# Performance work log

Measured on AMD Instinct MI355X. Metric: run time of the kernel, lower is better.

Reference implementation:

```python
import jax, jax.numpy as jnp
import numpy as np

B, CIN, H, W = 16, 3, 128, 128
C = 256          # out_channels
NH = 8           # num_heads
HD = C // NH     # head_dim = 32
SCALE = HD ** -0.5
EPS = 1e-5


def setup_inputs() -> dict:
    key = jax.random.key(0)
    ks = jax.random.split(key, 8)
    def xavier(k, fan_out, fan_in):
        lim = np.sqrt(6.0 / (fan_in + fan_out))
        return jax.random.uniform(k, (fan_out, fan_in), jnp.float32, -lim, lim)
    return {
        "x": jax.random.normal(ks[0], (B, CIN, H, W), jnp.float32),
        "Wi": xavier(ks[1], C, CIN),      # input_conv 1x1
        "bi": jnp.zeros((C,), jnp.float32),
        "Wqkv": xavier(ks[2], 3 * C, C),  # qkv_conv 1x1, no bias
        "Wo": xavier(ks[3], C, C),        # output_proj
        "bo": jnp.zeros((C,), jnp.float32),
        "Wf": xavier(ks[4], C, C),        # feature_update_conv
        "bf": jnp.zeros((C,), jnp.float32),
        "gamma": jnp.ones((C,), jnp.float32),
        "beta": jnp.zeros((C,), jnp.float32),
        "rmean": jnp.zeros((C,), jnp.float32),
        "rvar": jnp.ones((C,), jnp.float32),
    }


def reference(x, Wi, bi, Wqkv, Wo, bo, Wf, bf, gamma, beta, rmean, rvar):
    b, _, h, w = x.shape
    hw = h * w
    # input 1x1 conv
    x1 = jnp.einsum('oi,bihw->bohw', Wi, x) + bi[:, None, None]
    # qkv 1x1 conv, reshape (b, NH, 3, HD, h*w) matching torch channel layout
    qkv = jnp.einsum('oi,bihw->bohw', Wqkv, x1).reshape(b, NH, 3, HD, hw)
    q, k, v = qkv[:, :, 0], qkv[:, :, 1], qkv[:, :, 2]  # each (b, NH, HD, hw)
    # channel-channel attention: (b, NH, HD, HD), sigmoid gate (no softmax)
    attention = jax.nn.sigmoid(jnp.einsum('bndp,bnep->bnde', q, k) * SCALE)
    A = jnp.einsum('bnde,bnep->bndp', attention, v).reshape(b, C, h, w)
    A = jnp.einsum('oi,bihw->bohw', Wo, A) + bo[:, None, None]
    A = jnp.einsum('oi,bihw->bohw', Wf, A) + bf[:, None, None]
    # BatchNorm2d (eval mode: running stats)
    inv = gamma / jnp.sqrt(rvar + EPS)
    A = (A - rmean[:, None, None]) * inv[:, None, None] + beta[:, None, None]
    A = jax.nn.silu(A)  # dropout is identity in eval
    out = A + x1
    return (out, attention)
```

## Files before the change

### kernel.cpp

```cpp
#include <hip/hip_runtime.h>
#include <math.h>


#define HW 16384
#define NBATCH 16
static constexpr float SCALE_ = 0.17677669529663687f;
static constexpr float EPS_ = 1e-5f;

#define WS_PART 0
#define WS_WFO  4096
#define WS_BFO  69632
#define WS_WB4  69888
#define WS_AQ   71168
#define WS_A4G  75776

__device__ __forceinline__ float sigmoidf_(float z) {
  return 1.0f / (1.0f + __expf(-z));
}

__global__ __launch_bounds__(256) void k_prep(
    const float* __restrict__ x,
    const float* __restrict__ Wi, const float* __restrict__ bi,
    const float* __restrict__ Wqkv,
    const float* __restrict__ Wo, const float* __restrict__ bo,
    const float* __restrict__ Wf, const float* __restrict__ bf,
    float* __restrict__ part, float* __restrict__ Wfo,
    float* __restrict__ bfo, float* __restrict__ Wb4,
    float* __restrict__ aqg)
{
  const int bx = blockIdx.x;
  const int tid = threadIdx.x;
  if (bx < 256) {
    const int b = bx >> 4;
    const int pi = bx & 15;
    const int p0 = pi * 1024 + tid * 4;
    const float4 a0 = *reinterpret_cast<const float4*>(x + (size_t)(b * 3 + 0) * HW + p0);
    const float4 a1 = *reinterpret_cast<const float4*>(x + (size_t)(b * 3 + 1) * HW + p0);
    const float4 a2 = *reinterpret_cast<const float4*>(x + (size_t)(b * 3 + 2) * HW + p0);
    float v[9];
    v[0] = a0.x * a0.x + a0.y * a0.y + a0.z * a0.z + a0.w * a0.w;
    v[1] = a0.x * a1.x + a0.y * a1.y + a0.z * a1.z + a0.w * a1.w;
    v[2] = a0.x * a2.x + a0.y * a2.y + a0.z * a2.z + a0.w * a2.w;
    v[3] = a1.x * a1.x + a1.y * a1.y + a1.z * a1.z + a1.w * a1.w;
    v[4] = a1.x * a2.x + a1.y * a2.y + a1.z * a2.z + a1.w * a2.w;
    v[5] = a2.x * a2.x + a2.y * a2.y + a2.z * a2.z + a2.w * a2.w;
    v[6] = a0.x + a0.y + a0.z + a0.w;
    v[7] = a1.x + a1.y + a1.z + a1.w;
    v[8] = a2.x + a2.y + a2.z + a2.w;
    __shared__ float wred[4][9];
    const int lane = tid & 63, wid = tid >> 6;
#pragma unroll
    for (int k = 0; k < 9; ++k) {
      float s = v[k];
#pragma unroll
      for (int off = 32; off; off >>= 1) s += __shfl_down(s, off, 64);
      if (lane == 0) wred[wid][k] = s;
    }
    __syncthreads();
    if (tid < 9) {
      part[bx * 9 + tid] = wred[0][tid] + wred[1][tid] + wred[2][tid] + wred[3][tid];
    }
  } else if (bx < 512) {
    const int o = bx - 256;
    const float* wfr = Wf + (size_t)o * 256;
    const int i = tid;
    float acc = 0.f;
#pragma unroll 32
    for (int k = 0; k < 256; ++k) acc = fmaf(wfr[k], Wo[(size_t)k * 256 + i], acc);
    Wfo[(size_t)o * 256 + i] = acc;
  } else if (bx == 512) {
    Wb4[tid * 4 + 0] = Wi[tid * 3 + 0];
    Wb4[tid * 4 + 1] = Wi[tid * 3 + 1];
    Wb4[tid * 4 + 2] = Wi[tid * 3 + 2];
    Wb4[tid * 4 + 3] = bi[tid];
    float acc = bf[tid];
    const float* wfr = Wf + (size_t)tid * 256;
#pragma unroll 16
    for (int k = 0; k < 256; ++k) acc = fmaf(wfr[k], bo[k], acc);
    bfo[tid] = acc;
  } else {
    const int blk = bx - 513;
    const int rl = tid >> 2;
    const int ch = tid & 3;
    const int row = blk * 64 + rl;
    const float* wr = Wqkv + (size_t)row * 256 + ch * 64;
    float c0 = 0, c1 = 0, c2 = 0, c3 = 0;
#pragma unroll 8
    for (int c = 0; c < 64; ++c) {
      const float w = wr[c];
      const int cc = ch * 64 + c;
      c0 = fmaf(w, Wi[cc * 3 + 0], c0);
      c1 = fmaf(w, Wi[cc * 3 + 1], c1);
      c2 = fmaf(w, Wi[cc * 3 + 2], c2);
      c3 = fmaf(w, bi[cc], c3);
    }
    __shared__ float red[64][4][4];
    red[rl][ch][0] = c0; red[rl][ch][1] = c1;
    red[rl][ch][2] = c2; red[rl][ch][3] = c3;
    __syncthreads();
    const int j = tid & 3;
    aqg[(size_t)(blk * 64 + rl) * 4 + j] =
        red[rl][0][j] + red[rl][1][j] + red[rl][2][j] + red[rl][3][j];
  }
}

__global__ __launch_bounds__(256) void k_solveA(
    const float* __restrict__ part, const float* __restrict__ aqg,
    float* __restrict__ att_out,
    float* __restrict__ A4g)
{
  const int n = blockIdx.x;
  const int b = blockIdx.y;
  const int tid = threadIdx.x;
  __shared__ float Ms[9];
  __shared__ float aqh[96][5];
  __shared__ float att_s[32][33];
  if (tid < 9) {
    float s = 0.f;
    for (int j = 0; j < 16; ++j) s += part[(b * 16 + j) * 9 + tid];
    Ms[tid] = s;
  }
  if (tid < 96) {
    const float4 v = *reinterpret_cast<const float4*>(aqg + (size_t)(n * 96 + tid) * 4);
    aqh[tid][0] = v.x; aqh[tid][1] = v.y; aqh[tid][2] = v.z; aqh[tid][3] = v.w;
  }
  __syncthreads();
  const float M00 = Ms[0], M01 = Ms[1], M02 = Ms[2], M11 = Ms[3], M12 = Ms[4], M22 = Ms[5];
  const float s0 = Ms[6], s1 = Ms[7], s2 = Ms[8];
#pragma unroll
  for (int r = 0; r < 4; ++r) {
    const int idx = tid + r * 256;
    const int d = idx >> 5, e = idx & 31;
    const float* q = aqh[d];
    const float* k = aqh[32 + e];
    const float q0 = q[0], q1 = q[1], q2 = q[2], q3 = q[3];
    const float k0 = k[0], k1 = k[1], k2 = k[2], k3 = k[3];
    const float t = q0 * (M00 * k0 + M01 * k1 + M02 * k2)
                  + q1 * (M01 * k0 + M11 * k1 + M12 * k2)
                  + q2 * (M02 * k0 + M12 * k1 + M22 * k2)
                  + q3 * (s0 * k0 + s1 * k1 + s2 * k2)
                  + k3 * (s0 * q0 + s1 * q1 + s2 * q2)
                  + 16384.0f * q3 * k3;
    const float a = sigmoidf_(SCALE_ * t);
    att_s[d][e] = a;
    att_out[(size_t)(b * 8 + n) * 1024 + idx] = a;
  }
  __syncthreads();
  if (tid < 128) {
    const int d = tid >> 2, j = tid & 3;
    float acc = 0.f;
#pragma unroll 8
    for (int e = 0; e < 32; ++e) acc = fmaf(att_s[d][e], aqh[64 + e][j], acc);
    A4g[(size_t)(b * 256 + n * 32 + d) * 4 + j] = acc;
  }
}

__global__ __launch_bounds__(256) void k_final(
    const float* __restrict__ x,
    const float* __restrict__ Wfo, const float* __restrict__ bfo,
    const float* __restrict__ A4g, const float4* __restrict__ Wb4,
    const float* __restrict__ gamma, const float* __restrict__ beta,
    const float* __restrict__ rmean, const float* __restrict__ rvar,
    float* __restrict__ out)
{
  const int b = blockIdx.z;
  const int c0 = blockIdx.y * 32;
  const int tid = threadIdx.x;
  __shared__ float4 A4v[256];
  __shared__ float Wfo_s[32][257];
  __shared__ float4 partial[32][9];
  __shared__ float4 gg_s[32];
  __shared__ float4 wb_s[32];

  A4v[tid] = *reinterpret_cast<const float4*>(A4g + ((size_t)b * 256 + tid) * 4);
#pragma unroll
  for (int it = 0; it < 8; ++it) {
    const int idx = tid + it * 256;
    const int r = idx >> 6, kq = idx & 63;
    const float4 v = *reinterpret_cast<const float4*>(
        Wfo + ((size_t)(c0 + r) * 256 + kq * 4));
    Wfo_s[r][kq * 4 + 0] = v.x; Wfo_s[r][kq * 4 + 1] = v.y;
    Wfo_s[r][kq * 4 + 2] = v.z; Wfo_s[r][kq * 4 + 3] = v.w;
  }
  __syncthreads();
  {
    const int ks = tid >> 5, o = tid & 31;
    float4 acc = make_float4(0.f, 0.f, 0.f, 0.f);
#pragma unroll 8
    for (int i = 0; i < 32; ++i) {
      const float w = Wfo_s[o][ks * 32 + i];
      const float4 a = A4v[ks * 32 + i];
      acc.x = fmaf(w, a.x, acc.x); acc.y = fmaf(w, a.y, acc.y);
      acc.z = fmaf(w, a.z, acc.z); acc.w = fmaf(w, a.w, acc.w);
    }
    partial[o][ks] = acc;
  }
  __syncthreads();
  if (tid < 32) {
    const int o = tid;
    float4 s = partial[o][0];
#pragma unroll
    for (int k2 = 1; k2 < 8; ++k2) {
      const float4 p = partial[o][k2];
      s.x += p.x; s.y += p.y; s.z += p.z; s.w += p.w;
    }
    const int c = c0 + o;
    const float inv = gamma[c] / sqrtf(rvar[c] + EPS_);
    const float g3 = (s.w + bfo[c] - rmean[c]) * inv + beta[c];
    gg_s[o] = make_float4(s.x * inv, s.y * inv, s.z * inv, g3);
    wb_s[o] = Wb4[c];
  }
  __syncthreads();

  const int p4 = (blockIdx.x * 256 + tid) * 4;
  const float4 X0 = *reinterpret_cast<const float4*>(x + (size_t)(b * 3 + 0) * HW + p4);
  const float4 X1 = *reinterpret_cast<const float4*>(x + (size_t)(b * 3 + 1) * HW + p4);
  const float4 X2 = *reinterpret_cast<const float4*>(x + (size_t)(b * 3 + 2) * HW + p4);
  float* ob = out + (size_t)(b * 256 + c0) * HW + p4;
#pragma unroll 2
  for (int ci = 0; ci < 32; ++ci) {
    const float4 g = gg_s[ci];
    const float4 w = wb_s[ci];
    float4 r;
    {
      const float y = fmaf(g.x, X0.x, fmaf(g.y, X1.x, fmaf(g.z, X2.x, g.w)));
      r.x = y * sigmoidf_(y) + fmaf(w.x, X0.x, fmaf(w.y, X1.x, fmaf(w.z, X2.x, w.w)));
    }
    {
      const float y = fmaf(g.x, X0.y, fmaf(g.y, X1.y, fmaf(g.z, X2.y, g.w)));
      r.y = y * sigmoidf_(y) + fmaf(w.x, X0.y, fmaf(w.y, X1.y, fmaf(w.z, X2.y, w.w)));
    }
    {
      const float y = fmaf(g.x, X0.z, fmaf(g.y, X1.z, fmaf(g.z, X2.z, g.w)));
      r.z = y * sigmoidf_(y) + fmaf(w.x, X0.z, fmaf(w.y, X1.z, fmaf(w.z, X2.z, w.w)));
    }
    {
      const float y = fmaf(g.x, X0.w, fmaf(g.y, X1.w, fmaf(g.z, X2.w, g.w)));
      r.w = y * sigmoidf_(y) + fmaf(w.x, X0.w, fmaf(w.y, X1.w, fmaf(w.z, X2.w, w.w)));
    }
    *reinterpret_cast<float4*>(ob) = r;
    ob += HW;
  }
}

extern "C" void kernel_launch(void* const* d_in, const int* in_sizes, int n_in,
                              void* d_out, int out_size, void* d_ws, size_t ws_size,
                              hipStream_t stream) {
  const float* x     = (const float*)d_in[0];
  const float* Wi    = (const float*)d_in[1];
  const float* bi    = (const float*)d_in[2];
  const float* Wqkv  = (const float*)d_in[3];
  const float* Wo    = (const float*)d_in[4];
  const float* bo    = (const float*)d_in[5];
  const float* Wf    = (const float*)d_in[6];
  const float* bf    = (const float*)d_in[7];
  const float* gamma = (const float*)d_in[8];
  const float* beta  = (const float*)d_in[9];
  const float* rmean = (const float*)d_in[10];
  const float* rvar  = (const float*)d_in[11];

  float* out = (float*)d_out;
  float* att = out + (size_t)NBATCH * 256 * HW;
  float* wsf = (float*)d_ws;

  k_prep<<<dim3(525), dim3(256), 0, stream>>>(x, Wi, bi, Wqkv, Wo, bo, Wf, bf,
                                              wsf + WS_PART, wsf + WS_WFO,
                                              wsf + WS_BFO, wsf + WS_WB4,
                                              wsf + WS_AQ);
  k_solveA<<<dim3(8, NBATCH), dim3(256), 0, stream>>>(wsf + WS_PART, wsf + WS_AQ,
                                                      att, wsf + WS_A4G);
  k_final<<<dim3(16, 8, NBATCH), dim3(256), 0, stream>>>(
      x, wsf + WS_WFO, wsf + WS_BFO, wsf + WS_A4G,
      (const float4*)(wsf + WS_WB4), gamma, beta, rmean, rvar, out);
}
```

Baseline: 70.69 us.

## Split per-batch channel folding into separate kernel and streamline final write kernel

The per-(batch, channel-group) reduction of Wfo against A4 was recomputed in each of 16 spatial blocks of the final kernel. It now runs once in a new k_fold kernel that writes folded coefficients to workspace. The final kernel becomes one block per (channel, batch) that streams all pixels with nontemporal stores, removing the redundant smem GEMV and its barriers. The cost is an extra kernel launch and the x input being re-read once per output channel, which should mostly hit in cache.

```diff
diff --git a/kernel.cpp b/kernel.cpp
--- a/kernel.cpp
+++ b/kernel.cpp
@@ -6,6 +6,8 @@
 #define NBATCH 16
 static constexpr float SCALE_ = 0.17677669529663687f;
 static constexpr float EPS_ = 1e-5f;
+
+typedef float f32x4 __attribute__((ext_vector_type(4)));
 
 #define WS_PART 0
 #define WS_WFO  4096
@@ -13,6 +15,7 @@
 #define WS_WB4  69888
 #define WS_AQ   71168
 #define WS_A4G  75776
+#define WS_GG   92160
 
 __device__ __forceinline__ float sigmoidf_(float z) {
   return 1.0f / (1.0f + __expf(-z));
@@ -155,22 +158,19 @@
   }
 }
 
-__global__ __launch_bounds__(256) void k_final(
-    const float* __restrict__ x,
+__global__ __launch_bounds__(256) void k_fold(
     const float* __restrict__ Wfo, const float* __restrict__ bfo,
-    const float* __restrict__ A4g, const float4* __restrict__ Wb4,
+    const float* __restrict__ A4g,
     const float* __restrict__ gamma, const float* __restrict__ beta,
     const float* __restrict__ rmean, const float* __restrict__ rvar,
-    float* __restrict__ out)
-{
-  const int b = blockIdx.z;
-  const int c0 = blockIdx.y * 32;
+    float* __restrict__ Gg)
+{
+  const int c0 = blockIdx.x * 32;
+  const int b = blockIdx.y;
   const int tid = threadIdx.x;
   __shared__ float4 A4v[256];
   __shared__ float Wfo_s[32][257];
   __shared__ float4 partial[32][9];
-  __shared__ float4 gg_s[32];
-  __shared__ float4 wb_s[32];
 
   A4v[tid] = *reinterpret_cast<const float4*>(A4g + ((size_t)b * 256 + tid) * 4);
 #pragma unroll
@@ -207,21 +207,31 @@
     const int c = c0 + o;
     const float inv = gamma[c] / sqrtf(rvar[c] + EPS_);
     const float g3 = (s.w + bfo[c] - rmean[c]) * inv + beta[c];
-    gg_s[o] = make_float4(s.x * inv, s.y * inv, s.z * inv, g3);
-    wb_s[o] = Wb4[c];
-  }
-  __syncthreads();
-
-  const int p4 = (blockIdx.x * 256 + tid) * 4;
-  const float4 X0 = *reinterpret_cast<const float4*>(x + (size_t)(b * 3 + 0) * HW + p4);
-  const float4 X1 = *reinterpret_cast<const float4*>(x + (size_t)(b * 3 + 1) * HW + p4);
-  const float4 X2 = *reinterpret_cast<const float4*>(x + (size_t)(b * 3 + 2) * HW + p4);
-  float* ob = out + (size_t)(b * 256 + c0) * HW + p4;
-#pragma unroll 2
-  for (int ci = 0; ci < 32; ++ci) {
-    const float4 g = gg_s[ci];
-    const float4 w = wb_s[ci];
-    float4 r;
+    *reinterpret_cast<float4*>(Gg + (size_t)(b * 256 + c) * 4) =
+        make_float4(s.x * inv, s.y * inv, s.z * inv, g3);
+  }
+}
+
+__global__ __launch_bounds__(256) void k_final(
+    const float* __restrict__ x,
+    const float4* __restrict__ Gg4,
+    const float4* __restrict__ Wb4,
+    float* __restrict__ out)
+{
+  const int c = blockIdx.x;
+  const int b = blockIdx.y;
+  const float4 g = Gg4[b * 256 + c];
+  const float4 w = Wb4[c];
+  const float* xb = x + (size_t)b * 3 * HW;
+  float* ob = out + ((size_t)b * 256 + c) * HW;
+  const int t4 = threadIdx.x * 4;
+#pragma unroll 4
+  for (int it = 0; it < 16; ++it) {
+    const int p = it * 1024 + t4;
+    const float4 X0 = *reinterpret_cast<const float4*>(xb + p);
+    const float4 X1 = *reinterpret_cast<const float4*>(xb + HW + p);
+    const float4 X2 = *reinterpret_cast<const float4*>(xb + 2 * HW + p);
+    f32x4 r;
     {
       const float y = fmaf(g.x, X0.x, fmaf(g.y, X1.x, fmaf(g.z, X2.x, g.w)));
       r.x = y * sigmoidf_(y) + fmaf(w.x, X0.x, fmaf(w.y, X1.x, fmaf(w.z, X2.x, w.w)));
@@ -238,8 +248,7 @@
       const float y = fmaf(g.x, X0.w, fmaf(g.y, X1.w, fmaf(g.z, X2.w, g.w)));
       r.w = y * sigmoidf_(y) + fmaf(w.x, X0.w, fmaf(w.y, X1.w, fmaf(w.z, X2.w, w.w)));
     }
-    *reinterpret_cast<float4*>(ob) = r;
-    ob += HW;
+    __builtin_nontemporal_store(r, reinterpret_cast<f32x4*>(ob + p));
   }
 }
 
@@ -269,7 +278,9 @@
                                               wsf + WS_AQ);
   k_solveA<<<dim3(8, NBATCH), dim3(256), 0, stream>>>(wsf + WS_PART, wsf + WS_AQ,
                                                       att, wsf + WS_A4G);
-  k_final<<<dim3(16, 8, NBATCH), dim3(256), 0, stream>>>(
-      x, wsf + WS_WFO, wsf + WS_BFO, wsf + WS_A4G,
-      (const float4*)(wsf + WS_WB4), gamma, beta, rmean, rvar, out);
-}
+  k_fold<<<dim3(8, NBATCH), dim3(256), 0, stream>>>(wsf + WS_WFO, wsf + WS_BFO,
+                                                    wsf + WS_A4G, gamma, beta,
+                                                    rmean, rvar, wsf + WS_GG);
+  k_final<<<dim3(256, NBATCH), dim3(256), 0, stream>>>(
+      x, (const float4*)(wsf + WS_GG), (const float4*)(wsf + WS_WB4), out);
+}
```

After: 76.56 us. 8.3% more time.
